# Performance work log

Measured on AMD Instinct MI355X. Metric: run time of the kernel, lower is better.

Reference implementation:

```python
import jax, jax.numpy as jnp
import numpy as np

HID = 16
F_IN = 9
NUM_GRAPHS = 1000
EPS = 1e-5
NEG_SLOPE = 0.2


def _gat_conv(x, src, dst, W, a_src, a_dst, b):
    # GATConv, heads=1: h = x W; e_ij = LeakyReLU(a_src.h_j + a_dst.h_i); softmax over incoming edges of i
    N = x.shape[0]
    h = x @ W                                  # [N, HID]
    alpha_s = h @ a_src                        # [N]
    alpha_d = h @ a_dst                        # [N]
    e = jax.nn.leaky_relu(alpha_s[src] + alpha_d[dst], NEG_SLOPE)  # [E]
    m = jax.ops.segment_max(e, dst, num_segments=N)
    a = jnp.exp(e - m[dst])
    s = jax.ops.segment_sum(a, dst, num_segments=N)
    a = a / s[dst]                             # self-loops guarantee s > 0
    out = jax.ops.segment_sum(a[:, None] * h[src], dst, num_segments=N)
    return out + b


def _graph_norm(x, batch, w, b, mean_scale):
    cnt = jax.ops.segment_sum(jnp.ones((x.shape[0],), x.dtype), batch, num_segments=NUM_GRAPHS)[:, None]
    mean = jax.ops.segment_sum(x, batch, num_segments=NUM_GRAPHS) / cnt
    sub = x - mean_scale * mean[batch]
    var = jax.ops.segment_sum(sub * sub, batch, num_segments=NUM_GRAPHS) / cnt
    return w * sub / jnp.sqrt(var[batch] + EPS) + b


def setup_inputs() -> dict:
    key = jax.random.key(0)
    ks = jax.random.split(key, 32)
    N, E = 500_000, 5_000_000
    inp = {
        "x": jax.random.normal(ks[0], (N, F_IN), jnp.float32),
        "edge_index": jax.random.randint(ks[1], (2, E), 0, N, dtype=jnp.int64) if jax.config.jax_enable_x64 else jax.random.randint(ks[1], (2, E), 0, N, dtype=jnp.int32),
        "batch": jnp.sort(jax.random.randint(ks[2], (N,), 0, NUM_GRAPHS, dtype=jnp.int32)),
        "edge_weight": jax.random.uniform(ks[3], (E,), jnp.float32),
    }
    dims = [F_IN, HID, HID, HID]
    for i in range(4):
        d_in = dims[i]
        k = jax.random.split(ks[4 + i], 7)
        sc = 1.0 / np.sqrt(d_in)
        inp[f"W{i+1}"] = jax.random.normal(k[0], (d_in, HID), jnp.float32) * sc
        inp[f"asrc{i+1}"] = jax.random.normal(k[1], (HID,), jnp.float32) * 0.25
        inp[f"adst{i+1}"] = jax.random.normal(k[2], (HID,), jnp.float32) * 0.25
        inp[f"b{i+1}"] = jnp.zeros((HID,), jnp.float32)
        inp[f"gw{i+1}"] = jnp.ones((HID,), jnp.float32)
        inp[f"gb{i+1}"] = jnp.zeros((HID,), jnp.float32)
        inp[f"ga{i+1}"] = jnp.ones((HID,), jnp.float32)  # mean_scale
    inp["lin_w"] = jax.random.normal(ks[30], (HID, 2), jnp.float32) * (1.0 / np.sqrt(HID))
    inp["lin_b"] = jnp.zeros((2,), jnp.float32)
    return inp


def reference(x, edge_index, batch, edge_weight,
              W1, asrc1, adst1, b1, gw1, gb1, ga1,
              W2, asrc2, adst2, b2, gw2, gb2, ga2,
              W3, asrc3, adst3, b3, gw3, gb3, ga3,
              W4, asrc4, adst4, b4, gw4, gb4, ga4,
              lin_w, lin_b):
    # eval mode: dropout / dropout_edge / feat_mask are identity.
    # edge_weight is passed to GATConv but ignored (edge_dim=None in PyG GATConv).
    N = x.shape[0]
    loops = jnp.arange(N, dtype=edge_index.dtype)
    src = jnp.concatenate([edge_index[0], loops])  # add_self_loops=True (GATConv default)
    dst = jnp.concatenate([edge_index[1], loops])

    x1 = jax.nn.relu(_graph_norm(_gat_conv(x, src, dst, W1, asrc1, adst1, b1), batch, gw1, gb1, ga1))
    h2 = _graph_norm(_gat_conv(x1, src, dst, W2, asrc2, adst2, b2), batch, gw2, gb2, ga2)
    x2 = jax.nn.relu(h2 + x1)
    h3 = _graph_norm(_gat_conv(x2, src, dst, W3, asrc3, adst3, b3), batch, gw3, gb3, ga3)
    x3 = jax.nn.relu(h3 + x2)
    h4 = _graph_norm(_gat_conv(x3, src, dst, W4, asrc4, adst4, b4), batch, gw4, gb4, ga4)
    x4 = jax.nn.relu(h4 + x3)

    pooled = jax.ops.segment_sum(x4, batch, num_segments=NUM_GRAPHS)
    cnt = jax.ops.segment_sum(jnp.ones((N,), x4.dtype), batch, num_segments=NUM_GRAPHS)
    pooled = pooled / cnt[:, None]
    return pooled @ lin_w + lin_b
```

## Files before the change

### kernel.cpp

```cpp
#include <hip/hip_runtime.h>
#include <hip/hip_bf16.h>

#define HID 16
#define NGRAPH 1000
#define NEG_SLOPE 0.2f
#define EPS_GN 1e-5f
#define BSH 11
#define BS 2048
#define NBMAX 2048
#define CHK 4096
#define SRCB (32 - BSH)
#define RBITS 3
#define NRANGE 8
#define PADBKT 6400


typedef __hip_bfloat16 bf16;

static __device__ __forceinline__ float b2f(bf16 v) { return __bfloat162float(v); }

static __device__ __forceinline__ unsigned int pack2(float a, float b) {
    unsigned int ia = __float_as_uint(a);
    unsigned int ib = __float_as_uint(b);
    ia += 0x7FFFu + ((ia >> 16) & 1u);
    ib += 0x7FFFu + ((ib >> 16) & 1u);
    return (ia >> 16) | (ib & 0xFFFF0000u);
}

static __device__ __forceinline__ void fma_row(const uint4 ra, const uint4 rb, float p,
                                               float* __restrict__ acc) {
    unsigned int us[8] = {ra.x, ra.y, ra.z, ra.w, rb.x, rb.y, rb.z, rb.w};
#pragma unroll
    for (int q = 0; q < 8; ++q) {
        float lo = __uint_as_float(us[q] << 16);
        float hi = __uint_as_float(us[q] & 0xFFFF0000u);
        acc[2 * q]     = fmaf(p, lo, acc[2 * q]);
        acc[2 * q + 1] = fmaf(p, hi, acc[2 * q + 1]);
    }
}

static __device__ __forceinline__ float dot16(const uint4 ra, const uint4 rb,
                                              const float* __restrict__ w) {
    unsigned int us[8] = {ra.x, ra.y, ra.z, ra.w, rb.x, rb.y, rb.z, rb.w};
    float a = 0.f;
#pragma unroll
    for (int q = 0; q < 8; ++q) {
        float lo = __uint_as_float(us[q] << 16);
        float hi = __uint_as_float(us[q] & 0xFFFF0000u);
        a = fmaf(lo, w[2 * q], a);
        a = fmaf(hi, w[2 * q + 1], a);
    }
    return a;
}

struct PtrPack { const void* src[30]; int cnt[30]; int dstoff[30]; int n; };

__global__ void detect_cvt(const void* x, const void* ei, int* flags, PtrPack pk,
                           float* __restrict__ dst) {
    __shared__ int cbf, czero;
    __shared__ int isbS;
    int t = threadIdx.x;
    if (t == 0) { cbf = 0; czero = 0; }
    __syncthreads();
    const unsigned int* xw = (const unsigned int*)x;
    unsigned int w = xw[t * 4];
    int e_lo = (int)((w >> 7) & 0xFF);
    if (e_lo >= 100 && e_lo <= 140) atomicAdd(&cbf, 1);
    const unsigned int* ew = (const unsigned int*)ei;
    if (ew[2 * t + 1] == 0u) atomicAdd(&czero, 1);
    __syncthreads();
    if (t == 0) {
        int isb = (cbf >= 192) ? 1 : 0;
        flags[0] = isb;
        flags[1] = (czero >= 250) ? 1 : 0;
        isbS = isb;
    }
    __syncthreads();
    int isb = isbS;
    for (int j = 0; j < pk.n; ++j) {
        const void* s = pk.src[j];
        int c = pk.cnt[j], o = pk.dstoff[j];
        for (int i = t; i < c; i += blockDim.x) {
            float v = isb ? b2f(((const bf16*)s)[i]) : ((const float*)s)[i];
            dst[o + i] = v;
        }
    }
}

static __device__ __forceinline__ int ld_src(const int* ei, int E, int e, int i64) {
    return i64 ? ei[2ll * e] : ei[e];
}
static __device__ __forceinline__ int ld_dst(const int* ei, int E, int e, int i64) {
    return i64 ? ei[2ll * (E + e)] : ei[(long long)E + e];
}


__global__ void bucket_count(const int* __restrict__ ei, int E, const int* __restrict__ flags,
                             int* __restrict__ bcnt, int NB) {
    __shared__ int lh[NBMAX];
    int tid = threadIdx.x;
    for (int i = tid; i < NB; i += 256) lh[i] = 0;
    __syncthreads();
    int i64 = flags[1];
    int stride = gridDim.x * 256;
    for (int e = blockIdx.x * 256 + tid; e < E; e += stride)
        atomicAdd(&lh[ld_dst(ei, E, e, i64) >> BSH], 1);
    __syncthreads();
    for (int i = tid; i < NB; i += 256)
        if (lh[i]) atomicAdd(&bcnt[i], lh[i]);
}

__global__ void scan_buckets(const int* __restrict__ bcnt, int NB, int E,
                             int* __restrict__ gBase, int* __restrict__ gCursor) {
    __shared__ int part[256];
    int t = threadIdx.x;
    int per = (NB + 255) >> 8;
    int lo = t * per, hi = min(lo + per, NB);
    int s = 0;
    for (int i = lo; i < hi; ++i) s += bcnt[i];
    part[t] = s;
    __syncthreads();
    for (int off = 1; off < 256; off <<= 1) {
        int v = (t >= off) ? part[t - off] : 0;
        __syncthreads();
        part[t] += v;
        __syncthreads();
    }
    int acc = (t == 0) ? 0 : part[t - 1];
    for (int i = lo; i < hi; ++i) {
        gBase[i] = acc; gCursor[i] = acc;
        acc += bcnt[i];
    }
    if (t == 0) gBase[NB] = E;
}

__global__ void bucket_scatter(const int* __restrict__ ei, int E, const int* __restrict__ flags,
                               int* __restrict__ gCursor, unsigned int* __restrict__ binned,
                               int NB) {
    __shared__ int lh[NBMAX];
    __shared__ int lbase[NBMAX];
    __shared__ int lcur[NBMAX];
    int tid = threadIdx.x;
    int i64 = flags[1];
    int nchunk = (E + CHK - 1) / CHK;
    for (int chunk = blockIdx.x; chunk < nchunk; chunk += gridDim.x) {
        int c0 = chunk * CHK;
        int c1 = min(c0 + CHK, E);
        for (int i = tid; i < NB; i += 256) lh[i] = 0;
        __syncthreads();
        for (int e = c0 + tid; e < c1; e += 256)
            atomicAdd(&lh[ld_dst(ei, E, e, i64) >> BSH], 1);
        __syncthreads();
        for (int b = tid; b < NB; b += 256) {
            int c = lh[b];
            lbase[b] = c ? atomicAdd(&gCursor[b], c) : 0;
            lcur[b] = 0;
        }
        __syncthreads();
        for (int e = c0 + tid; e < c1; e += 256) {
            int d = ld_dst(ei, E, e, i64);
            int s = ld_src(ei, E, e, i64);
            int b = d >> BSH;
            int off = atomicAdd(&lcur[b], 1);
            binned[lbase[b] + off] = ((unsigned)(d & (BS - 1)) << SRCB) | (unsigned)s;
        }
        __syncthreads();
    }
}

__global__ void bucket_sort(const unsigned int* __restrict__ binned, const int* __restrict__ gBase,
                            int* __restrict__ csrPad, int* __restrict__ rowPadBase,
                            int* __restrict__ rowCnt, int N, int srcShift) {
    __shared__ int hist[BS * NRANGE];
    __shared__ int tsum[1024];
    int tid = threadIdx.x;
    int b = blockIdx.x;
    int base = gBase[b];
    int cnt = gBase[b + 1] - base;
    int padBase = ((base + 3) & ~3) + PADBKT * b;
    for (int i = tid; i < BS * NRANGE; i += 1024) hist[i] = 0;
    __syncthreads();
    for (int i = tid; i < cnt; i += 1024) {
        unsigned int w = binned[base + i];
        int dstLow = (int)(w >> SRCB);
        int src = (int)(w & ((1u << SRCB) - 1u));
        atomicAdd(&hist[(dstLow << RBITS) | (src >> srcShift)], 1);
    }
    __syncthreads();
    int c[2 * NRANGE];
    int t0 = tid * (2 * NRANGE);
    int cnt0 = 0, cnt1 = 0;
#pragma unroll
    for (int i = 0; i < NRANGE; ++i) { c[i] = hist[t0 + i]; cnt0 += c[i]; }
#pragma unroll
    for (int i = NRANGE; i < 2 * NRANGE; ++i) { c[i] = hist[t0 + i]; cnt1 += c[i]; }
    int pad0 = (cnt0 + 3) & ~3;
    int pad1 = (cnt1 + 3) & ~3;
    tsum[tid] = pad0 + pad1;
    __syncthreads();
    for (int off = 1; off < 1024; off <<= 1) {
        int v = (tid >= off) ? tsum[tid - off] : 0;
        __syncthreads();
        tsum[tid] += v;
        __syncthreads();
    }
    int excl = (tid == 0) ? 0 : tsum[tid - 1];
    int ab0 = padBase + excl;
    int ab1 = ab0 + pad0;
    int d0 = b * BS + 2 * tid;
    if (d0 < N)     { rowPadBase[d0] = ab0;     rowCnt[d0] = cnt0; }
    if (d0 + 1 < N) { rowPadBase[d0 + 1] = ab1; rowCnt[d0 + 1] = cnt1; }
    int run = ab0;
#pragma unroll
    for (int i = 0; i < NRANGE; ++i) { hist[t0 + i] = run; run += c[i]; }
    run = ab1;
#pragma unroll
    for (int i = NRANGE; i < 2 * NRANGE; ++i) { hist[t0 + i] = run; run += c[i]; }
    __syncthreads();
    for (int i = tid; i < cnt; i += 1024) {
        unsigned int w = binned[base + i];
        int dstLow = (int)(w >> SRCB);
        int src = (int)(w & ((1u << SRCB) - 1u));
        int key = (dstLow << RBITS) | (src >> srcShift);
        int off = atomicAdd(&hist[key], 1);
        csrPad[off] = src;
    }
    __syncthreads();
    if (d0 < N && cnt0 > 0 && pad0 > cnt0) {
        int last = csrPad[ab0 + cnt0 - 1];
        for (int i = cnt0; i < pad0; ++i) csrPad[ab0 + i] = last;
    }
    if (d0 + 1 < N && cnt1 > 0 && pad1 > cnt1) {
        int last = csrPad[ab1 + cnt1 - 1];
        for (int i = cnt1; i < pad1; ++i) csrPad[ab1 + i] = last;
    }
}

__global__ void graph_cnt_k(const int* __restrict__ batch, int N, float* __restrict__ gcnt) {
    int g = blockIdx.x * blockDim.x + threadIdx.x;
    if (g < NGRAPH) {
        int lo = 0, hi = N;
        while (lo < hi) { int mid = (lo + hi) >> 1; if (batch[mid] < g) lo = mid + 1; else hi = mid; }
        int lb = lo;
        lo = 0; hi = N;
        while (lo < hi) { int mid = (lo + hi) >> 1; if (batch[mid] <= g) lo = mid + 1; else hi = mid; }
        gcnt[g] = (float)(lo - lb);
    }
}

__global__ void node_feat0(const void* __restrict__ xin, int din,
                           const int* __restrict__ flags, const float* __restrict__ prmL,
                           unsigned int* __restrict__ hb, int N) {
    __shared__ float sW[256];
    int t = threadIdx.x;
    if (t < din * HID) sW[t] = prmL[t];
    __syncthreads();
    int i = blockIdx.x * blockDim.x + t;
    if (i >= N) return;
    int isb = flags[0];
    const float* xf = (const float*)xin;
    const bf16* xb16 = (const bf16*)xin;
    float hr[HID];
#pragma unroll
    for (int j = 0; j < HID; ++j) hr[j] = 0.f;
    int base = i * din;
    for (int k = 0; k < din; ++k) {
        float xv = isb ? b2f(xb16[base + k]) : xf[base + k];
#pragma unroll
        for (int j = 0; j < HID; ++j) hr[j] = fmaf(xv, sW[k * HID + j], hr[j]);
    }
    uint4* hp = (uint4*)(hb + ((size_t)i << 3));
    uint4 w0, w1;
    w0.x = pack2(hr[0], hr[1]);   w0.y = pack2(hr[2], hr[3]);
    w0.z = pack2(hr[4], hr[5]);   w0.w = pack2(hr[6], hr[7]);
    w1.x = pack2(hr[8], hr[9]);   w1.y = pack2(hr[10], hr[11]);
    w1.z = pack2(hr[12], hr[13]); w1.w = pack2(hr[14], hr[15]);
    hp[0] = w0; hp[1] = w1;
}

__global__ void __launch_bounds__(256, 4)
gat_agg(const int* __restrict__ rowPadBase, const int* __restrict__ rowCnt,
        const int* __restrict__ csrPad,
        const unsigned int* __restrict__ hb,
        const float* __restrict__ prmL, const int* __restrict__ batch,
        unsigned int* __restrict__ tb, float* __restrict__ gsum,
        float* __restrict__ gsumsq, int N) {
    __shared__ float sv[256][HID + 1];
    __shared__ int sg[256];
    int tid = threadIdx.x;
    int node = blockIdx.x * 256 + tid;
    bool valid = node < N;
    float acc[HID];
    float tv[HID];
    int g = -1;
    if (valid) {
        int pb = rowPadBase[node];
        int cnt = rowCnt[node];
        const uint4* hs = (const uint4*)(hb + ((size_t)node << 3));
        uint4 rs0 = hs[0], rs1 = hs[1];
        float asv = dot16(rs0, rs1, prmL + 256);
        float adi = dot16(rs0, rs1, prmL + 272);
        float zs = asv + adi;
        float e_self = zs > 0.f ? zs : NEG_SLOPE * zs;
        float m = e_self, ssum = 1.f;
        {
            unsigned int us[8] = {rs0.x, rs0.y, rs0.z, rs0.w, rs1.x, rs1.y, rs1.z, rs1.w};
#pragma unroll
            for (int qq = 0; qq < 8; ++qq) {
                acc[2 * qq]     = __uint_as_float(us[qq] << 16);
                acc[2 * qq + 1] = __uint_as_float(us[qq] & 0xFFFF0000u);
            }
        }
        uint4 si;
        if (cnt > 0) si = *(const uint4*)(csrPad + pb);
        for (int q = 0; q < cnt; q += 4) {
            int s0 = (int)si.x, s1 = (int)si.y, s2 = (int)si.z, s3 = (int)si.w;
            const uint4* h0 = (const uint4*)(hb + ((size_t)s0 << 3));
            const uint4* h1 = (const uint4*)(hb + ((size_t)s1 << 3));
            const uint4* h2 = (const uint4*)(hb + ((size_t)s2 << 3));
            const uint4* h3 = (const uint4*)(hb + ((size_t)s3 << 3));
            uint4 r00 = h0[0], r01 = h0[1];
            uint4 r10 = h1[0], r11 = h1[1];
            uint4 r20 = h2[0], r21 = h2[1];
            uint4 r30 = h3[0], r31 = h3[1];
            if (q + 4 < cnt) si = *(const uint4*)(csrPad + pb + q + 4);
            float a0 = dot16(r00, r01, prmL + 256);
            float a1 = dot16(r10, r11, prmL + 256);
            float a2 = dot16(r20, r21, prmL + 256);
            float a3 = dot16(r30, r31, prmL + 256);
            int k = cnt - q;
            float z0 = a0 + adi, z1 = a1 + adi, z2 = a2 + adi, z3 = a3 + adi;
            float e0 = z0 > 0.f ? z0 : NEG_SLOPE * z0;
            float e1 = (1 < k) ? (z1 > 0.f ? z1 : NEG_SLOPE * z1) : -1e30f;
            float e2 = (2 < k) ? (z2 > 0.f ? z2 : NEG_SLOPE * z2) : -1e30f;
            float e3 = (3 < k) ? (z3 > 0.f ? z3 : NEG_SLOPE * z3) : -1e30f;
            float cm = fmaxf(fmaxf(e0, e1), fmaxf(e2, e3));
            if (cm > m) {
                float sc = __expf(m - cm);
                ssum *= sc;
#pragma unroll
                for (int f = 0; f < HID; ++f) acc[f] *= sc;
                m = cm;
            }
            float p0 = __expf(e0 - m);
            float p1 = __expf(e1 - m);
            float p2 = __expf(e2 - m);
            float p3 = __expf(e3 - m);
            ssum += p0 + p1 + p2 + p3;
            fma_row(r00, r01, p0, acc);
            fma_row(r10, r11, p1, acc);
            fma_row(r20, r21, p2, acc);
            fma_row(r30, r31, p3, acc);
        }
        float inv = 1.f / ssum;
#pragma unroll
        for (int f = 0; f < HID; ++f) tv[f] = fmaf(acc[f], inv, prmL[288 + f]);
        uint4* tp = (uint4*)(tb + ((size_t)node << 3));
        uint4 w0, w1;
        w0.x = pack2(tv[0], tv[1]);   w0.y = pack2(tv[2], tv[3]);
        w0.z = pack2(tv[4], tv[5]);   w0.w = pack2(tv[6], tv[7]);
        w1.x = pack2(tv[8], tv[9]);   w1.y = pack2(tv[10], tv[11]);
        w1.z = pack2(tv[12], tv[13]); w1.w = pack2(tv[14], tv[15]);
        tp[0] = w0; tp[1] = w1;
        g = batch[node];
    }
    sg[tid] = valid ? g : -1;
#pragma unroll
    for (int f = 0; f < HID; ++f) sv[tid][f] = valid ? tv[f] : 0.f;
    __syncthreads();
    if (tid < 64) {
        int f = tid & 15;
        int seg = tid >> 4;
        int n0 = seg * 64, n1 = n0 + 64;
        float s1 = 0.f, s2 = 0.f;
        int cur = -2;
        for (int n = n0; n < n1; ++n) {
            int bg = sg[n];
            if (bg < 0) continue;
            if (bg != cur) {
                if (cur >= 0) { atomicAdd(&gsum[cur * HID + f], s1); atomicAdd(&gsumsq[cur * HID + f], s2); }
                cur = bg; s1 = 0.f; s2 = 0.f;
            }
            float v = sv[n][f];
            s1 += v; s2 += v * v;
        }
        if (cur >= 0) { atomicAdd(&gsum[cur * HID + f], s1); atomicAdd(&gsumsq[cur * HID + f], s2); }
    }
}

__global__ void norm_feat(const unsigned int* __restrict__ tb,
                          const float* __restrict__ gsum, const float* __restrict__ gsumsq,
                          const float* __restrict__ gcnt, const int* __restrict__ batch,
                          unsigned int* __restrict__ xb, int N, int residual, int isLast,
                          const float* __restrict__ prmL, const float* __restrict__ prmNext,
                          unsigned int* __restrict__ hb, float* __restrict__ pooled) {
    __shared__ float sW[256];
    __shared__ float sgw[HID], sgb[HID], sga[HID];
    __shared__ float sv[256][HID + 1];
    __shared__ int sg[256];
    int tid = threadIdx.x;
    if (!isLast) sW[tid] = prmNext[tid];
    if (tid < HID) { sgw[tid] = prmL[304 + tid]; sgb[tid] = prmL[320 + tid]; sga[tid] = prmL[336 + tid]; }
    __syncthreads();
    int i = blockIdx.x * 256 + tid;
    float v[HID];
    int g = -1;
    if (i < N) {
        g = batch[i];
        float invc = 1.f / gcnt[g];
        const uint4* tp = (const uint4*)(tb + ((size_t)i << 3));
        uint4 u0 = tp[0], u1 = tp[1];
        unsigned int us[8] = {u0.x, u0.y, u0.z, u0.w, u1.x, u1.y, u1.z, u1.w};
        float ts[HID];
#pragma unroll
        for (int q = 0; q < 8; ++q) {
            ts[2 * q]     = __uint_as_float(us[q] << 16);
            ts[2 * q + 1] = __uint_as_float(us[q] & 0xFFFF0000u);
        }
        float xs[HID];
        if (residual) {
            const uint4* xp = (const uint4*)(xb + ((size_t)i << 3));
            uint4 y0 = xp[0], y1 = xp[1];
            unsigned int uy[8] = {y0.x, y0.y, y0.z, y0.w, y1.x, y1.y, y1.z, y1.w};
#pragma unroll
            for (int q = 0; q < 8; ++q) {
                xs[2 * q]     = __uint_as_float(uy[q] << 16);
                xs[2 * q + 1] = __uint_as_float(uy[q] & 0xFFFF0000u);
            }
        } else {
#pragma unroll
            for (int f = 0; f < HID; ++f) xs[f] = 0.f;
        }
        const float4* s1p = (const float4*)(gsum + g * HID);
        const float4* s2p = (const float4*)(gsumsq + g * HID);
        float4 sa4[4], sb4[4];
#pragma unroll
        for (int q = 0; q < 4; ++q) { sa4[q] = s1p[q]; sb4[q] = s2p[q]; }
        float s1v[HID], s2v[HID];
#pragma unroll
        for (int q = 0; q < 4; ++q) {
            s1v[q*4+0] = sa4[q].x; s1v[q*4+1] = sa4[q].y; s1v[q*4+2] = sa4[q].z; s1v[q*4+3] = sa4[q].w;
            s2v[q*4+0] = sb4[q].x; s2v[q*4+1] = sb4[q].y; s2v[q*4+2] = sb4[q].z; s2v[q*4+3] = sb4[q].w;
        }
#pragma unroll
        for (int f = 0; f < HID; ++f) {
            float mean = s1v[f] * invc;
            float msq = s2v[f] * invc;
            float ga = sga[f];
            float var = msq + (ga * ga - 2.f * ga) * mean * mean;
            var = fmaxf(var, 0.f);
            float A = sgw[f] * rsqrtf(var + EPS_GN);
            float B = sgb[f] - A * ga * mean;
            float val = fmaf(A, ts[f], B) + xs[f];
            v[f] = fmaxf(val, 0.f);
        }
    }
    if (isLast) {
        sg[tid] = (i < N) ? g : -1;
#pragma unroll
        for (int f = 0; f < HID; ++f) sv[tid][f] = (i < N) ? v[f] : 0.f;
        __syncthreads();
        if (tid < 64) {
            int f = tid & 15;
            int seg = tid >> 4;
            int n0 = seg * 64, n1 = n0 + 64;
            float s1 = 0.f;
            int cur = -2;
            for (int n = n0; n < n1; ++n) {
                int bg = sg[n];
                if (bg < 0) continue;
                if (bg != cur) { if (cur >= 0) atomicAdd(&pooled[cur * HID + f], s1); cur = bg; s1 = 0.f; }
                s1 += sv[n][f];
            }
            if (cur >= 0) atomicAdd(&pooled[cur * HID + f], s1);
        }
    } else if (i < N) {
        uint4* xp = (uint4*)(xb + ((size_t)i << 3));
        uint4 y0, y1;
        y0.x = pack2(v[0], v[1]);   y0.y = pack2(v[2], v[3]);
        y0.z = pack2(v[4], v[5]);   y0.w = pack2(v[6], v[7]);
        y1.x = pack2(v[8], v[9]);   y1.y = pack2(v[10], v[11]);
        y1.z = pack2(v[12], v[13]); y1.w = pack2(v[14], v[15]);
        xp[0] = y0; xp[1] = y1;
        float hr[HID];
#pragma unroll
        for (int j = 0; j < HID; ++j) hr[j] = 0.f;
#pragma unroll
        for (int k = 0; k < HID; ++k) {
            float xv = v[k];
#pragma unroll
            for (int j = 0; j < HID; ++j) hr[j] = fmaf(xv, sW[k * HID + j], hr[j]);
        }
        uint4* hp = (uint4*)(hb + ((size_t)i << 3));
        uint4 w0, w1;
        w0.x = pack2(hr[0], hr[1]);   w0.y = pack2(hr[2], hr[3]);
        w0.z = pack2(hr[4], hr[5]);   w0.w = pack2(hr[6], hr[7]);
        w1.x = pack2(hr[8], hr[9]);   w1.y = pack2(hr[10], hr[11]);
        w1.z = pack2(hr[12], hr[13]); w1.w = pack2(hr[14], hr[15]);
        hp[0] = w0; hp[1] = w1;
    }
}

__global__ void final_lin(const float* __restrict__ pooled, const float* __restrict__ gcnt,
                          const float* __restrict__ prm, const int* __restrict__ flags,
                          void* __restrict__ out) {
    int g = blockIdx.x * blockDim.x + threadIdx.x;
    if (g < NGRAPH) {
        float c = gcnt[g];
        float invc = c > 0.f ? 1.f / c : 0.f;
        float o0 = prm[1440], o1 = prm[1441];
#pragma unroll
        for (int f = 0; f < HID; ++f) {
            float p = pooled[g * HID + f] * invc;
            o0 = fmaf(p, prm[1408 + f * 2 + 0], o0);
            o1 = fmaf(p, prm[1408 + f * 2 + 1], o1);
        }
        if (flags[0]) {
            ((bf16*)out)[g * 2 + 0] = __float2bfloat16(o0);
            ((bf16*)out)[g * 2 + 1] = __float2bfloat16(o1);
        } else {
            ((float*)out)[g * 2 + 0] = o0;
            ((float*)out)[g * 2 + 1] = o1;
        }
    }
}

extern "C" void kernel_launch(void* const* d_in, const int* in_sizes, int n_in,
                              void* d_out, int out_size, void* d_ws, size_t ws_size,
                              hipStream_t stream) {
    const void* x = d_in[0];
    const int* ei = (const int*)d_in[1];
    const int* batch = (const int*)d_in[2];
    int N = in_sizes[2];
    int E = in_sizes[1] / 2;
    int din0 = in_sizes[0] / N;
    int NB = (N + BS - 1) / BS;

    int srcShift = 0;
    while (((N - 1) >> srcShift) > (NRANGE - 1)) ++srcShift;

    int csrPadLen = ((E + 3) & ~3) + PADBKT * NB + 64;

    float* ws = (float*)d_ws;
    int* flags = (int*)ws;
    float* prm = ws + 16;
    unsigned int* hb = (unsigned int*)(ws + 4096);
    unsigned int* tb = hb + (size_t)N * 8;
    unsigned int* xb = tb + (size_t)N * 8;
    int* rowPadBase = (int*)(xb + (size_t)N * 8);
    int* rowCnt = rowPadBase + N;
    int* gBase = rowCnt + N;
    int* gCursor = gBase + NBMAX + 1;
    int* csrPad = gCursor + NBMAX;
    int* bcnt = csrPad + csrPadLen;
    float* gstat = (float*)(bcnt + NBMAX);
    float* pooled = gstat + 4 * 2 * NGRAPH * HID;
    float* gcnt = pooled + NGRAPH * HID;
    unsigned int* binned = (unsigned int*)hb;

    PtrPack pk;
    int n = 0;
    for (int l = 0; l < 4; ++l) {
        int dl = (l == 0) ? din0 : HID;
        int base = l * 352;
        const int offs[7] = {0, 256, 272, 288, 304, 320, 336};
        const int cnts[7] = {dl * HID, HID, HID, HID, HID, HID, HID};
        for (int j = 0; j < 7; ++j) {
            pk.src[n] = d_in[4 + l * 7 + j];
            pk.cnt[n] = cnts[j];
            pk.dstoff[n] = base + offs[j];
            ++n;
        }
    }
    pk.src[n] = d_in[32]; pk.cnt[n] = HID * 2; pk.dstoff[n] = 1408; ++n;
    pk.src[n] = d_in[33]; pk.cnt[n] = 2;       pk.dstoff[n] = 1440; ++n;
    pk.n = n;

    int nbN = (N + 255) / 256;
    int nchunk = (E + CHK - 1) / CHK;
    int scatterGrid = nchunk < 2048 ? nchunk : 2048;

    detect_cvt<<<1, 256, 0, stream>>>(x, ei, flags, pk, prm);

    size_t zbytes = (size_t)(NBMAX + 4 * 2 * NGRAPH * HID + NGRAPH * HID) * sizeof(int);
    hipMemsetAsync(bcnt, 0, zbytes, stream);

    bucket_count<<<1024, 256, 0, stream>>>(ei, E, flags, bcnt, NB);
    scan_buckets<<<1, 256, 0, stream>>>(bcnt, NB, E, gBase, gCursor);
    bucket_scatter<<<scatterGrid, 256, 0, stream>>>(ei, E, flags, gCursor, binned, NB);
    bucket_sort<<<NB, 1024, 0, stream>>>(binned, gBase, csrPad, rowPadBase, rowCnt, N, srcShift);
    graph_cnt_k<<<(NGRAPH + 255) / 256, 256, 0, stream>>>(batch, N, gcnt);

    node_feat0<<<nbN, 256, 0, stream>>>(x, din0, flags, prm, hb, N);

    for (int l = 0; l < 4; ++l) {
        const float* prmL = prm + l * 352;
        const float* prmNext = prm + (l + 1 < 4 ? (l + 1) * 352 : 0);
        float* gsumL = gstat + l * 2 * NGRAPH * HID;
        float* gsumsqL = gsumL + NGRAPH * HID;

        gat_agg<<<nbN, 256, 0, stream>>>(rowPadBase, rowCnt, csrPad, hb, prmL, batch,
                                         tb, gsumL, gsumsqL, N);
        norm_feat<<<nbN, 256, 0, stream>>>(tb, gsumL, gsumsqL, gcnt, batch, xb, N,
                                           l > 0 ? 1 : 0, l == 3 ? 1 : 0, prmL, prmNext,
                                           hb, pooled);
    }

    final_lin<<<(NGRAPH + 255) / 256, 256, 0, stream>>>(pooled, gcnt, prm, flags, d_out);
}
```

Baseline: 883.3 us.

## Stage bucket scatter in LDS for coalesced global writes

The bucket scatter kernel now sorts each chunk's packed edges into shared memory, using a per-chunk prefix scan of bucket counts, and then writes them to global memory in contiguous runs per bucket instead of as random scattered stores. The chunk size doubles and the grid is capped lower so each block stages more edges per pass. This adds a block-wide scan, extra shared-memory traffic and higher LDS use per block, which can reduce occupancy. With about 250 buckets, each run in a chunk averages only about 30 elements.

```diff
diff --git a/kernel.cpp b/kernel.cpp
--- a/kernel.cpp
+++ b/kernel.cpp
@@ -8,7 +8,7 @@
 #define BSH 11
 #define BS 2048
 #define NBMAX 2048
-#define CHK 4096
+#define CHK 8192
 #define SRCB (32 - BSH)
 #define RBITS 3
 #define NRANGE 8
@@ -137,32 +137,58 @@
 __global__ void bucket_scatter(const int* __restrict__ ei, int E, const int* __restrict__ flags,
                                int* __restrict__ gCursor, unsigned int* __restrict__ binned,
                                int NB) {
-    __shared__ int lh[NBMAX];
-    __shared__ int lbase[NBMAX];
-    __shared__ int lcur[NBMAX];
+    extern __shared__ int sm[];
+    unsigned int* staged = (unsigned int*)sm;
+    int* lh    = sm + CHK;
+    int* lbase = lh + NB;
+    int* lcur  = lbase + NB;
+    int* lofs  = lcur + NB;
+    __shared__ int part[256];
     int tid = threadIdx.x;
     int i64 = flags[1];
     int nchunk = (E + CHK - 1) / CHK;
     for (int chunk = blockIdx.x; chunk < nchunk; chunk += gridDim.x) {
         int c0 = chunk * CHK;
         int c1 = min(c0 + CHK, E);
-        for (int i = tid; i < NB; i += 256) lh[i] = 0;
+        int cn = c1 - c0;
+        for (int i = tid; i < NB; i += 256) { lh[i] = 0; lcur[i] = 0; }
         __syncthreads();
         for (int e = c0 + tid; e < c1; e += 256)
             atomicAdd(&lh[ld_dst(ei, E, e, i64) >> BSH], 1);
         __syncthreads();
-        for (int b = tid; b < NB; b += 256) {
-            int c = lh[b];
-            lbase[b] = c ? atomicAdd(&gCursor[b], c) : 0;
-            lcur[b] = 0;
-        }
+        int per = (NB + 255) >> 8;
+        int lo = tid * per, hi2 = min(lo + per, NB);
+        int s = 0;
+        for (int i = lo; i < hi2; ++i) s += lh[i];
+        part[tid] = s;
+        __syncthreads();
+        for (int off = 1; off < 256; off <<= 1) {
+            int v = (tid >= off) ? part[tid - off] : 0;
+            __syncthreads();
+            part[tid] += v;
+            __syncthreads();
+        }
+        int acc = (tid == 0) ? 0 : part[tid - 1];
+        for (int i = lo; i < hi2; ++i) {
+            int c = lh[i];
+            lofs[i] = acc;
+            lbase[i] = c ? atomicAdd(&gCursor[i], c) : 0;
+            acc += c;
+        }
+        if (tid == 0) lofs[NB] = cn;
         __syncthreads();
         for (int e = c0 + tid; e < c1; e += 256) {
             int d = ld_dst(ei, E, e, i64);
-            int s = ld_src(ei, E, e, i64);
+            int sct = ld_src(ei, E, e, i64);
             int b = d >> BSH;
             int off = atomicAdd(&lcur[b], 1);
-            binned[lbase[b] + off] = ((unsigned)(d & (BS - 1)) << SRCB) | (unsigned)s;
+            staged[lofs[b] + off] = ((unsigned)(d & (BS - 1)) << SRCB) | (unsigned)sct;
+        }
+        __syncthreads();
+        int b = 0;
+        for (int t = tid; t < cn; t += 256) {
+            while (t >= lofs[b + 1]) ++b;
+            binned[lbase[b] + (t - lofs[b])] = staged[t];
         }
         __syncthreads();
     }
@@ -578,7 +604,8 @@
 
     int nbN = (N + 255) / 256;
     int nchunk = (E + CHK - 1) / CHK;
-    int scatterGrid = nchunk < 2048 ? nchunk : 2048;
+    int scatterGrid = nchunk < 1024 ? nchunk : 1024;
+    size_t scatterLds = (size_t)(CHK + 4 * NB + 1) * sizeof(int);
 
     detect_cvt<<<1, 256, 0, stream>>>(x, ei, flags, pk, prm);
 
@@ -587,7 +614,7 @@
 
     bucket_count<<<1024, 256, 0, stream>>>(ei, E, flags, bcnt, NB);
     scan_buckets<<<1, 256, 0, stream>>>(bcnt, NB, E, gBase, gCursor);
-    bucket_scatter<<<scatterGrid, 256, 0, stream>>>(ei, E, flags, gCursor, binned, NB);
+    bucket_scatter<<<scatterGrid, 256, scatterLds, stream>>>(ei, E, flags, gCursor, binned, NB);
     bucket_sort<<<NB, 1024, 0, stream>>>(binned, gBase, csrPad, rowPadBase, rowCnt, N, srcShift);
     graph_cnt_k<<<(NGRAPH + 255) / 256, 256, 0, stream>>>(batch, N, gcnt);
 
```

Measured after the change: 839.0 us. 5.0% less time.
